# Kernel optimization log

Hardware: AMD Instinct MI355X
Metric: run time of the kernel (lower is better)

The kernel has to match this reference:

```python
import jax, jax.numpy as jnp
import numpy as np

B = 2048      # number of sequences with non-empty history
S = 32        # seq_len (all sequences full length for static shapes)
H = 256       # h_dim == embd_rank (ent/rel embedding dim)
NSEG = B * S  # total history timesteps (segments)
NNBR = 524288 # total gathered neighbor embeddings (avg 8 per segment)
ENT = 100000
REL = 1000


def setup_inputs() -> dict:
    key = jax.random.key(0)
    k1, k2, k3, k4, k5, k6, k7 = jax.random.split(key, 7)
    return {
        "neighbor_idx": jax.random.randint(k1, (NNBR,), 0, ENT),
        "segment_ids": jnp.sort(jax.random.randint(k2, (NNBR,), 0, NSEG)),
        "s_tem": jax.random.randint(k3, (B,), 0, ENT),
        "r_tem": jax.random.randint(k4, (B,), 0, REL),
        "s_hist_dt": jax.random.uniform(k5, (NSEG,), dtype=jnp.float32),
        "ent_embeds": jax.random.normal(k6, (ENT, H), dtype=jnp.float32),
        "rel_embeds": jax.random.normal(k7, (REL, H), dtype=jnp.float32),
    }


def reference(neighbor_idx, segment_ids, s_tem, r_tem, s_hist_dt, ent_embeds, rel_embeds):
    # gather neighbor entity embeddings (embeds_stack in the original)
    embeds_stack = ent_embeds[neighbor_idx]                     # [NNBR, H]
    # sparse.mm(mask, embeds_stack) == segment sum over neighbor groups
    sums = jax.ops.segment_sum(embeds_stack, segment_ids, num_segments=NSEG)
    counts = jax.ops.segment_sum(jnp.ones((NNBR,), embeds_stack.dtype),
                                 segment_ids, num_segments=NSEG)
    embeds_mean = sums / jnp.maximum(counts, 1.0)[:, None]      # [NSEG, H]
    # scatter means into padded [B, S, H] (all sequences full length)
    mean_seq = embeds_mean.reshape(B, S, H)
    # repeat subject entity / relation embeddings along time and concat
    ent_b = jnp.broadcast_to(ent_embeds[s_tem][:, None, :], (B, S, H))
    rel_b = jnp.broadcast_to(rel_embeds[r_tem][:, None, :], (B, S, H))
    s_embed_seq = jnp.concatenate([mean_seq, ent_b, rel_b], axis=-1)  # [B, S, 3H]
    s_hist_dt_seq = s_hist_dt.reshape(B, S)
    return s_embed_seq, s_hist_dt_seq
```

## Files before the change

### kernel.cpp

```cpp
#include <hip/hip_runtime.h>
#include <hip/hip_bf16.h>

#define BB    2048
#define SS    32
#define HH    256
#define NSEGC 65536
#define NNBRC 524288

__global__ __launch_bounds__(256) void seg_bounds_kernel(
    const int* __restrict__ segment_ids,
    int* __restrict__ start)
{
    const int seg = blockIdx.x * blockDim.x + threadIdx.x;
    if (seg > NSEGC) return;
    int lo = 0, hi = NNBRC;
    while (lo < hi) {
        const int mid = (lo + hi) >> 1;
        if (segment_ids[mid] < seg) lo = mid + 1;
        else hi = mid;
    }
    start[seg] = lo;
}

__global__ __launch_bounds__(256) void agg_kernel(
    const int*   __restrict__ neighbor_idx,
    const int*   __restrict__ s_tem,
    const int*   __restrict__ r_tem,
    const float* __restrict__ ent,
    const float* __restrict__ rel,
    const int*   __restrict__ start,
    float*       __restrict__ out)
{
    const int wave = (blockIdx.x * blockDim.x + threadIdx.x) >> 6;
    const int lane = threadIdx.x & 63;
    if (wave >= NSEGC) return;
    const int seg = wave;
    const int b   = seg >> 5;

    const int begin = start[seg];
    const int end   = start[seg + 1];

    float ax = 0.f, ay = 0.f, az = 0.f, aw = 0.f;

    for (int base = begin; base < end; base += 64) {
        const int cnt = min(64, end - base);
        int myidx = 0;
        if (lane < cnt) myidx = neighbor_idx[base + lane];
        #pragma unroll 4
        for (int j = 0; j < cnt; ++j) {
            const int nbr = __shfl(myidx, j);
            const float4 v = *reinterpret_cast<const float4*>(
                ent + (size_t)nbr * HH + lane * 4);
            ax += v.x; ay += v.y; az += v.z; aw += v.w;
        }
    }

    const float inv = 1.0f / fmaxf((float)(end - begin), 1.0f);
    float4 m;
    m.x = ax * inv; m.y = ay * inv; m.z = az * inv; m.w = aw * inv;

    float* o = out + (size_t)seg * (3 * HH);
    *reinterpret_cast<float4*>(o + lane * 4) = m;

    const int e = s_tem[b];
    const float4 ev = *reinterpret_cast<const float4*>(
        ent + (size_t)e * HH + lane * 4);
    *reinterpret_cast<float4*>(o + HH + lane * 4) = ev;

    const int r = r_tem[b];
    const float4 rv = *reinterpret_cast<const float4*>(
        rel + (size_t)r * HH + lane * 4);
    *reinterpret_cast<float4*>(o + 2 * HH + lane * 4) = rv;
}

__global__ __launch_bounds__(256) void dt_copy_kernel(
    const float* __restrict__ dt,
    float* __restrict__ out_tail)
{
    const int i = blockIdx.x * blockDim.x + threadIdx.x;
    reinterpret_cast<float4*>(out_tail)[i] =
        reinterpret_cast<const float4*>(dt)[i];
}

extern "C" void kernel_launch(void* const* d_in, const int* in_sizes, int n_in,
                              void* d_out, int out_size, void* d_ws, size_t ws_size,
                              hipStream_t stream) {
    const int*   neighbor_idx = (const int*)  d_in[0];
    const int*   segment_ids  = (const int*)  d_in[1];
    const int*   s_tem        = (const int*)  d_in[2];
    const int*   r_tem        = (const int*)  d_in[3];
    const float* s_hist_dt    = (const float*)d_in[4];
    const float* ent_embeds   = (const float*)d_in[5];
    const float* rel_embeds   = (const float*)d_in[6];
    float*       out          = (float*)d_out;

    int* start = (int*)d_ws;

    {
        const int threads = 256;
        const int total   = NSEGC + 1;
        const int blocks  = (total + threads - 1) / threads;
        seg_bounds_kernel<<<blocks, threads, 0, stream>>>(segment_ids, start);
    }

    {
        const int threads = 256;
        const int blocks  = NSEGC / 4;
        agg_kernel<<<blocks, threads, 0, stream>>>(
            neighbor_idx, s_tem, r_tem, ent_embeds, rel_embeds, start, out);
    }

    {
        float* out_tail = out + (size_t)NSEGC * (3 * HH);
        dt_copy_kernel<<<64, 256, 0, stream>>>(s_hist_dt, out_tail);
    }
}
```

Baseline: 345.9 us.

## Fuse dt copy into bounds kernel, remap blocks per XCD, use nontemporal stores

Folds the s_hist_dt copy into the segment-bounds kernel, which removes one kernel launch. It remaps workgroup indices so each of the 8 XCDs handles a contiguous range of segments, aiming for better L2 locality. The large output writes now use nontemporal stores so that write-once data does not pollute the cache and the L2 stays available for the gathered embedding rows. The remapping assumes the grid size divides evenly by 8.

```diff
diff --git a/kernel.cpp b/kernel.cpp
--- a/kernel.cpp
+++ b/kernel.cpp
@@ -6,20 +6,31 @@
 #define HH    256
 #define NSEGC 65536
 #define NNBRC 524288
+#define NXCD  8
 
-__global__ __launch_bounds__(256) void seg_bounds_kernel(
-    const int* __restrict__ segment_ids,
-    int* __restrict__ start)
+using f32x4 = __attribute__((ext_vector_type(4))) float;
+
+__global__ __launch_bounds__(256) void seg_bounds_dt_kernel(
+    const int*   __restrict__ segment_ids,
+    int*         __restrict__ start,
+    const float* __restrict__ dt,
+    float*       __restrict__ out_tail)
 {
-    const int seg = blockIdx.x * blockDim.x + threadIdx.x;
-    if (seg > NSEGC) return;
+    const int i = blockIdx.x * blockDim.x + threadIdx.x;
+
+    if (i < NSEGC / 4) {
+        const f32x4 v = reinterpret_cast<const f32x4*>(dt)[i];
+        __builtin_nontemporal_store(v, reinterpret_cast<f32x4*>(out_tail) + i);
+    }
+
+    if (i > NSEGC) return;
     int lo = 0, hi = NNBRC;
     while (lo < hi) {
         const int mid = (lo + hi) >> 1;
-        if (segment_ids[mid] < seg) lo = mid + 1;
+        if (segment_ids[mid] < i) lo = mid + 1;
         else hi = mid;
     }
-    start[seg] = lo;
+    start[i] = lo;
 }
 
 __global__ __launch_bounds__(256) void agg_kernel(
@@ -31,11 +42,13 @@
     const int*   __restrict__ start,
     float*       __restrict__ out)
 {
-    const int wave = (blockIdx.x * blockDim.x + threadIdx.x) >> 6;
+    const int chunk = gridDim.x / NXCD;
+    const int wg    = (blockIdx.x % NXCD) * chunk + blockIdx.x / NXCD;
+
+    const int seg  = wg * 4 + (threadIdx.x >> 6);
     const int lane = threadIdx.x & 63;
-    if (wave >= NSEGC) return;
-    const int seg = wave;
-    const int b   = seg >> 5;
+    if (seg >= NSEGC) return;
+    const int b = seg >> 5;
 
     const int begin = start[seg];
     const int end   = start[seg + 1];
@@ -49,37 +62,28 @@
         #pragma unroll 4
         for (int j = 0; j < cnt; ++j) {
             const int nbr = __shfl(myidx, j);
-            const float4 v = *reinterpret_cast<const float4*>(
+            const f32x4 v = *reinterpret_cast<const f32x4*>(
                 ent + (size_t)nbr * HH + lane * 4);
             ax += v.x; ay += v.y; az += v.z; aw += v.w;
         }
     }
 
     const float inv = 1.0f / fmaxf((float)(end - begin), 1.0f);
-    float4 m;
+    f32x4 m;
     m.x = ax * inv; m.y = ay * inv; m.z = az * inv; m.w = aw * inv;
 
     float* o = out + (size_t)seg * (3 * HH);
-    *reinterpret_cast<float4*>(o + lane * 4) = m;
+    __builtin_nontemporal_store(m, reinterpret_cast<f32x4*>(o) + lane);
 
     const int e = s_tem[b];
-    const float4 ev = *reinterpret_cast<const float4*>(
+    const f32x4 ev = *reinterpret_cast<const f32x4*>(
         ent + (size_t)e * HH + lane * 4);
-    *reinterpret_cast<float4*>(o + HH + lane * 4) = ev;
+    __builtin_nontemporal_store(ev, reinterpret_cast<f32x4*>(o + HH) + lane);
 
     const int r = r_tem[b];
-    const float4 rv = *reinterpret_cast<const float4*>(
+    const f32x4 rv = *reinterpret_cast<const f32x4*>(
         rel + (size_t)r * HH + lane * 4);
-    *reinterpret_cast<float4*>(o + 2 * HH + lane * 4) = rv;
-}
-
-__global__ __launch_bounds__(256) void dt_copy_kernel(
-    const float* __restrict__ dt,
-    float* __restrict__ out_tail)
-{
-    const int i = blockIdx.x * blockDim.x + threadIdx.x;
-    reinterpret_cast<float4*>(out_tail)[i] =
-        reinterpret_cast<const float4*>(dt)[i];
+    __builtin_nontemporal_store(rv, reinterpret_cast<f32x4*>(o + 2 * HH) + lane);
 }
 
 extern "C" void kernel_launch(void* const* d_in, const int* in_sizes, int n_in,
@@ -100,7 +104,9 @@
         const int threads = 256;
         const int total   = NSEGC + 1;
         const int blocks  = (total + threads - 1) / threads;
-        seg_bounds_kernel<<<blocks, threads, 0, stream>>>(segment_ids, start);
+        float* out_tail = out + (size_t)NSEGC * (3 * HH);
+        seg_bounds_dt_kernel<<<blocks, threads, 0, stream>>>(
+            segment_ids, start, s_hist_dt, out_tail);
     }
 
     {
@@ -109,9 +115,4 @@
         agg_kernel<<<blocks, threads, 0, stream>>>(
             neighbor_idx, s_tem, r_tem, ent_embeds, rel_embeds, start, out);
     }
-
-    {
-        float* out_tail = out + (size_t)NSEGC * (3 * HH);
-        dt_copy_kernel<<<64, 256, 0, stream>>>(s_hist_dt, out_tail);
-    }
 }
```

Result: faster. 338.8 us (-2.0%).
